# Optimization experiments

Hardware: AMD Instinct MI355X
Metric: run time of the kernel (lower is better)

The kernel has to match this reference:

```python
import jax, jax.numpy as jnp
import numpy as np


def setup_inputs() -> dict:
    key = jax.random.key(0)
    k1, k2 = jax.random.split(key)
    N, D, E = 16384, 4096, 64  # tokens, n_embd, n_exp
    x = jax.random.normal(k1, (N, D), dtype=jnp.float32)
    W = jax.random.normal(k2, (E, D), dtype=jnp.float32) * 0.02  # w_gate weight [n_exp, n_embd]
    return {"x": x, "W": W, "top_k": 4, "n_groups": 8, "n_limited_groups": 4}


def reference(x, W, top_k, n_groups, n_limited_groups):
    ROUTE_SCALE = 1.0
    N = x.shape[0]
    E = W.shape[0]
    exp_per_group = E // n_groups

    logits = x @ W.T                      # [N, E] gate linear (bias=False)
    scores = jax.nn.softmax(logits, -1)   # func == 'softmax'

    # group-limited routing: pick top n_limited_groups groups by max score (bias=False path)
    gs = scores.reshape(N, n_groups, exp_per_group)
    group_scores = gs.max(axis=-1)                             # [N, G]
    _, top_grp = jax.lax.top_k(group_scores, n_limited_groups)  # [N, L]
    selected = jnp.any(
        jnp.arange(n_groups)[None, None, :] == top_grp[:, :, None], axis=1
    )                                                           # [N, G] bool
    masked = jnp.where(selected[:, :, None], gs, -jnp.inf).reshape(N, E)

    # top-k experts over unmasked scores; weights are the gathered scores
    topk_vals, topk_idx = jax.lax.top_k(masked, top_k)          # [N, K]
    weights = (topk_vals * ROUTE_SCALE).astype(x.dtype)         # softmax -> no renorm

    # histc over expert ids
    counts = jnp.zeros((E,), jnp.int32).at[topk_idx.reshape(-1)].add(1)
    return weights, topk_idx, counts
```

## Files before the change

### kernel.cpp

```cpp
#include <hip/hip_runtime.h>
#include <math.h>

#define NTOK 16384
#define DDIM 4096
#define NEXP 64
#define KTOP 4

#define BK   128
#define NSTG (DDIM / BK)
#define TPB  64
#define NBLK (NTOK / TPB)

typedef __attribute__((ext_vector_type(8))) short short8;
typedef __attribute__((ext_vector_type(4))) float f32x4;


__device__ __forceinline__ unsigned short f2bf_rtn(float x) {
    unsigned int b = __float_as_uint(x);
    return (unsigned short)((b + 0x7FFFu + ((b >> 16) & 1u)) >> 16);
}
__device__ __forceinline__ float bf2f(unsigned short h) {
    return __uint_as_float(((unsigned int)h) << 16);
}
__device__ __forceinline__ short8 mk8(unsigned int a, unsigned int b,
                                      unsigned int c, unsigned int d) {
    union { unsigned int u[4]; short8 s; } p;
    p.u[0] = a; p.u[1] = b; p.u[2] = c; p.u[3] = d;
    return p.s;
}
__device__ __forceinline__ void gl2lds16(const void* g, void* l) {
    __builtin_amdgcn_global_load_lds(
        (const __attribute__((address_space(1))) unsigned int*)g,
        (__attribute__((address_space(3))) unsigned int*)l, 16, 0, 0);
}

__global__ __launch_bounds__(256) void prep_kernel(
    const float* __restrict__ W, unsigned short* __restrict__ Whi,
    unsigned short* __restrict__ Wlo, float* __restrict__ counts)
{
    int idx = blockIdx.x * 256 + threadIdx.x;
    float x = W[idx];
    unsigned short h = f2bf_rtn(x);
    float lo = x - bf2f(h);
    Whi[idx] = h;
    Wlo[idx] = f2bf_rtn(lo);
    if (blockIdx.x == 0 && threadIdx.x < NEXP) counts[threadIdx.x] = 0.0f;
}

__global__ __launch_bounds__(512, 2) void gate_kernel(
    const float* __restrict__ X, const unsigned short* __restrict__ Whi,
    const unsigned short* __restrict__ Wlo, float* __restrict__ outW,
    float* __restrict__ outI, float* __restrict__ counts)
{
    __shared__ float          sX[2][TPB * BK];
    __shared__ unsigned short sH[2][NEXP * BK];
    __shared__ unsigned short sL[2][NEXP * BK];
    __shared__ float          lgt[TPB][66];
    __shared__ int            hist[NEXP];

    const int tid  = threadIdx.x;
    const int lane = tid & 63;
    const int w    = tid >> 6;
    const int wm   = w >> 2;
    const int wn   = w & 3;
    const int tok0 = blockIdx.x * TPB;

    if (tid < NEXP) hist[tid] = 0;

    const float* xsrc[4];
    int xdstf[4];
    #pragma unroll
    for (int i = 0; i < 4; ++i) {
        const int seg = w * 4 + i;
        const int r0  = seg * 2 + (lane >> 5);
        const int pc  = lane & 31;
        xsrc[i]  = X + (size_t)(tok0 + r0) * DDIM + ((pc ^ (r0 & 15)) * 4);
        xdstf[i] = seg * 256;
    }
    const unsigned short *whsrc[2], *wlsrc[2];
    int wdsts[2];
    #pragma unroll
    for (int j = 0; j < 2; ++j) {
        const int seg2 = w * 2 + j;
        const int e    = seg2 * 4 + (lane >> 4);
        const int sc   = lane & 15;
        const size_t o = (size_t)e * DDIM + ((sc ^ (e & 15)) * 8);
        whsrc[j] = Whi + o;
        wlsrc[j] = Wlo + o;
        wdsts[j] = seg2 * 512;
    }

    #pragma unroll
    for (int i = 0; i < 4; ++i) gl2lds16(xsrc[i], &sX[0][xdstf[i]]);
    #pragma unroll
    for (int j = 0; j < 2; ++j) {
        gl2lds16(whsrc[j], &sH[0][wdsts[j]]);
        gl2lds16(wlsrc[j], &sL[0][wdsts[j]]);
    }
    __syncthreads();

    const int fr = lane & 15;
    const int fg = lane >> 4;
    const int rowA0 = (wm * 32 + fr) * BK;
    const int rowA1 = rowA0 + 16 * BK;
    const int eB    = (wn * 16 + fr) * BK;

    f32x4 acc[2];
    acc[0] = (f32x4){0.f, 0.f, 0.f, 0.f};
    acc[1] = (f32x4){0.f, 0.f, 0.f, 0.f};

    for (int st = 0; st < NSTG; ++st) {
        const float*          cx = sX[st & 1];
        const unsigned short* ch = sH[st & 1];
        const unsigned short* cl = sL[st & 1];

        if (st + 1 < NSTG) {
            const int nb = (st + 1) & 1;
            const int ko = (st + 1) * BK;
            #pragma unroll
            for (int i = 0; i < 4; ++i)
                gl2lds16(xsrc[i] + ko, &sX[nb][xdstf[i]]);
            #pragma unroll
            for (int j = 0; j < 2; ++j) {
                gl2lds16(whsrc[j] + ko, &sH[nb][wdsts[j]]);
                gl2lds16(wlsrc[j] + ko, &sL[nb][wdsts[j]]);
            }
        }

        #pragma unroll
        for (int ks = 0; ks < 4; ++ks) {
            const int ch0 = ks * 8 + fg * 2;
            const float4 a00 = *(const float4*)&cx[rowA0 + ((ch0     ) ^ fr) * 4];
            const float4 a01 = *(const float4*)&cx[rowA0 + ((ch0 + 1) ^ fr) * 4];
            const float4 a10 = *(const float4*)&cx[rowA1 + ((ch0     ) ^ fr) * 4];
            const float4 a11 = *(const float4*)&cx[rowA1 + ((ch0 + 1) ^ fr) * 4];

            short8 ahi[2], alo[2];
            #pragma unroll
            for (int mg = 0; mg < 2; ++mg) {
                const float4 qa = mg ? a10 : a00;
                const float4 qb = mg ? a11 : a01;
                const unsigned int u0 = __float_as_uint(qa.x), u1 = __float_as_uint(qa.y);
                const unsigned int u2 = __float_as_uint(qa.z), u3 = __float_as_uint(qa.w);
                const unsigned int u4 = __float_as_uint(qb.x), u5 = __float_as_uint(qb.y);
                const unsigned int u6 = __float_as_uint(qb.z), u7 = __float_as_uint(qb.w);
                unsigned int hi0 = (u0 >> 16) | (u1 & 0xFFFF0000u);
                unsigned int hi1 = (u2 >> 16) | (u3 & 0xFFFF0000u);
                unsigned int hi2 = (u4 >> 16) | (u5 & 0xFFFF0000u);
                unsigned int hi3 = (u6 >> 16) | (u7 & 0xFFFF0000u);
                const float l0 = qa.x - __uint_as_float(u0 & 0xFFFF0000u);
                const float l1 = qa.y - __uint_as_float(u1 & 0xFFFF0000u);
                const float l2 = qa.z - __uint_as_float(u2 & 0xFFFF0000u);
                const float l3 = qa.w - __uint_as_float(u3 & 0xFFFF0000u);
                const float l4 = qb.x - __uint_as_float(u4 & 0xFFFF0000u);
                const float l5 = qb.y - __uint_as_float(u5 & 0xFFFF0000u);
                const float l6 = qb.z - __uint_as_float(u6 & 0xFFFF0000u);
                const float l7 = qb.w - __uint_as_float(u7 & 0xFFFF0000u);
                unsigned int lo0 = (__float_as_uint(l0) >> 16) | (__float_as_uint(l1) & 0xFFFF0000u);
                unsigned int lo1 = (__float_as_uint(l2) >> 16) | (__float_as_uint(l3) & 0xFFFF0000u);
                unsigned int lo2 = (__float_as_uint(l4) >> 16) | (__float_as_uint(l5) & 0xFFFF0000u);
                unsigned int lo3 = (__float_as_uint(l6) >> 16) | (__float_as_uint(l7) & 0xFFFF0000u);
                ahi[mg] = mk8(hi0, hi1, hi2, hi3);
                alo[mg] = mk8(lo0, lo1, lo2, lo3);
            }

            const int cb = (ks * 4 + fg) ^ fr;
            const short8 bh = *(const short8*)&ch[eB + cb * 8];
            const short8 bl = *(const short8*)&cl[eB + cb * 8];

            #pragma unroll
            for (int mg = 0; mg < 2; ++mg) {
                acc[mg] = __builtin_amdgcn_mfma_f32_16x16x32_bf16(ahi[mg], bh, acc[mg], 0, 0, 0);
                acc[mg] = __builtin_amdgcn_mfma_f32_16x16x32_bf16(ahi[mg], bl, acc[mg], 0, 0, 0);
                acc[mg] = __builtin_amdgcn_mfma_f32_16x16x32_bf16(alo[mg], bh, acc[mg], 0, 0, 0);
            }
        }

        __syncthreads();
    }

    #pragma unroll
    for (int mg = 0; mg < 2; ++mg)
        #pragma unroll
        for (int r = 0; r < 4; ++r)
            lgt[wm * 32 + mg * 16 + fg * 4 + r][wn * 16 + fr] = acc[mg][r];
    __syncthreads();

    for (int t = 0; t < 8; ++t) {
        const int nl = w * 8 + t;
        const int n  = tok0 + nl;
        const float L = lgt[nl][lane];

        float m = L;
        #pragma unroll
        for (int off = 32; off > 0; off >>= 1) m = fmaxf(m, __shfl_xor(m, off));
        float p = expf(L - m);
        float ssum = p;
        #pragma unroll
        for (int off = 32; off > 0; off >>= 1) ssum += __shfl_xor(ssum, off);
        const float score = p / ssum;

        float gm = score;
        gm = fmaxf(gm, __shfl_xor(gm, 1));
        gm = fmaxf(gm, __shfl_xor(gm, 2));
        gm = fmaxf(gm, __shfl_xor(gm, 4));

        float ga[8];
        #pragma unroll
        for (int g = 0; g < 8; ++g) ga[g] = __shfl(gm, g * 8);
        unsigned selmask = 0u;
        #pragma unroll
        for (int r = 0; r < 4; ++r) {
            float best = -INFINITY; int bg = 0;
            #pragma unroll
            for (int g = 0; g < 8; ++g) {
                bool taken  = (selmask >> g) & 1u;
                bool better = (!taken) && (ga[g] > best);
                bg   = better ? g : bg;
                best = better ? ga[g] : best;
            }
            selmask |= (1u << bg);
        }

        float ms = ((selmask >> (lane >> 3)) & 1u) ? score : -INFINITY;
        float wk[4]; int wi[4];
        #pragma unroll
        for (int r = 0; r < 4; ++r) {
            float v = ms; int ix = lane;
            #pragma unroll
            for (int off = 32; off > 0; off >>= 1) {
                float vo = __shfl_xor(v, off);
                int   io = __shfl_xor(ix, off);
                if (vo > v || (vo == v && io < ix)) { v = vo; ix = io; }
            }
            wk[r] = v; wi[r] = ix;
            if (lane == ix) ms = -INFINITY;
        }

        if (lane == 0) {
            *(float4*)&outW[(size_t)n * 4] = make_float4(wk[0], wk[1], wk[2], wk[3]);
            *(float4*)&outI[(size_t)n * 4] =
                make_float4((float)wi[0], (float)wi[1], (float)wi[2], (float)wi[3]);
            atomicAdd(&hist[wi[0]], 1);
            atomicAdd(&hist[wi[1]], 1);
            atomicAdd(&hist[wi[2]], 1);
            atomicAdd(&hist[wi[3]], 1);
        }
    }

    __syncthreads();
    if (tid < NEXP) atomicAdd(&counts[tid], (float)hist[tid]);
}

extern "C" void kernel_launch(void* const* d_in, const int* in_sizes, int n_in,
                              void* d_out, int out_size, void* d_ws, size_t ws_size,
                              hipStream_t stream) {
    const float* X = (const float*)d_in[0];
    const float* W = (const float*)d_in[1];

    float* outW   = (float*)d_out;
    float* outI   = outW + (size_t)NTOK * KTOP;
    float* counts = outW + (size_t)2 * NTOK * KTOP;

    unsigned short* Whi = (unsigned short*)d_ws;
    unsigned short* Wlo = Whi + (size_t)NEXP * DDIM;

    prep_kernel<<<(NEXP * DDIM) / 256, 256, 0, stream>>>(W, Whi, Wlo, counts);
    gate_kernel<<<NBLK, 512, 0, stream>>>(X, Whi, Wlo, outW, outI, counts);
}
```

Measured before the change: 120.3 us.

## Halve token tile and read bf16 gate weights directly from global memory

The token tile per block shrinks from 64 to 32, and occupancy is raised to four blocks per CU. The split hi/lo bf16 weight tiles are no longer staged through LDS; each lane loads its B fragments straight from global (L2-resident) memory. This frees LDS and cuts the async copy traffic so more blocks can be resident. In exchange, each weight fragment is reused across fewer tokens, and the MFMA loop now depends on global-load latency for B.

Result: slower. 154.4 us (+28.3%).

```diff
diff --git a/kernel.cpp b/kernel.cpp
--- a/kernel.cpp
+++ b/kernel.cpp
@@ -6,10 +6,10 @@
 #define NEXP 64
 #define KTOP 4
 
+#define TPB  32
+#define NBLK (NTOK / TPB)
 #define BK   128
 #define NSTG (DDIM / BK)
-#define TPB  64
-#define NBLK (NTOK / TPB)
 
 typedef __attribute__((ext_vector_type(8))) short short8;
 typedef __attribute__((ext_vector_type(4))) float f32x4;
@@ -47,16 +47,14 @@
     if (blockIdx.x == 0 && threadIdx.x < NEXP) counts[threadIdx.x] = 0.0f;
 }
 
-__global__ __launch_bounds__(512, 2) void gate_kernel(
+__global__ __launch_bounds__(512, 4) void gate_kernel(
     const float* __restrict__ X, const unsigned short* __restrict__ Whi,
     const unsigned short* __restrict__ Wlo, float* __restrict__ outW,
     float* __restrict__ outI, float* __restrict__ counts)
 {
-    __shared__ float          sX[2][TPB * BK];
-    __shared__ unsigned short sH[2][NEXP * BK];
-    __shared__ unsigned short sL[2][NEXP * BK];
-    __shared__ float          lgt[TPB][66];
-    __shared__ int            hist[NEXP];
+    __shared__ float sX[2][TPB * BK];
+    __shared__ float lgt[TPB][66];
+    __shared__ int   hist[NEXP];
 
     const int tid  = threadIdx.x;
     const int lane = tid & 63;
@@ -67,127 +65,86 @@
 
     if (tid < NEXP) hist[tid] = 0;
 
-    const float* xsrc[4];
-    int xdstf[4];
+    const float* xsrc[2];
+    int xdstf[2];
     #pragma unroll
-    for (int i = 0; i < 4; ++i) {
-        const int seg = w * 4 + i;
-        const int r0  = seg * 2 + (lane >> 5);
-        const int pc  = lane & 31;
-        xsrc[i]  = X + (size_t)(tok0 + r0) * DDIM + ((pc ^ (r0 & 15)) * 4);
-        xdstf[i] = seg * 256;
+    for (int i = 0; i < 2; ++i) {
+        const int r = w * 4 + i * 2 + (lane >> 5);
+        const int p = lane & 31;
+        xsrc[i]  = X + (size_t)(tok0 + r) * DDIM + ((p ^ (r & 15)) * 4);
+        xdstf[i] = w * 512 + i * 256;
     }
-    const unsigned short *whsrc[2], *wlsrc[2];
-    int wdsts[2];
-    #pragma unroll
-    for (int j = 0; j < 2; ++j) {
-        const int seg2 = w * 2 + j;
-        const int e    = seg2 * 4 + (lane >> 4);
-        const int sc   = lane & 15;
-        const size_t o = (size_t)e * DDIM + ((sc ^ (e & 15)) * 8);
-        whsrc[j] = Whi + o;
-        wlsrc[j] = Wlo + o;
-        wdsts[j] = seg2 * 512;
-    }
-
-    #pragma unroll
-    for (int i = 0; i < 4; ++i) gl2lds16(xsrc[i], &sX[0][xdstf[i]]);
-    #pragma unroll
-    for (int j = 0; j < 2; ++j) {
-        gl2lds16(whsrc[j], &sH[0][wdsts[j]]);
-        gl2lds16(wlsrc[j], &sL[0][wdsts[j]]);
-    }
+
+    gl2lds16(xsrc[0], &sX[0][xdstf[0]]);
+    gl2lds16(xsrc[1], &sX[0][xdstf[1]]);
     __syncthreads();
 
     const int fr = lane & 15;
     const int fg = lane >> 4;
-    const int rowA0 = (wm * 32 + fr) * BK;
-    const int rowA1 = rowA0 + 16 * BK;
-    const int eB    = (wn * 16 + fr) * BK;
-
-    f32x4 acc[2];
-    acc[0] = (f32x4){0.f, 0.f, 0.f, 0.f};
-    acc[1] = (f32x4){0.f, 0.f, 0.f, 0.f};
+    const int rowA = (wm * 16 + fr) * BK;
+    const unsigned short* wh = Whi + (size_t)(wn * 16 + fr) * DDIM + fg * 8;
+    const unsigned short* wl = Wlo + (size_t)(wn * 16 + fr) * DDIM + fg * 8;
+
+    f32x4 acc = (f32x4){0.f, 0.f, 0.f, 0.f};
 
     for (int st = 0; st < NSTG; ++st) {
-        const float*          cx = sX[st & 1];
-        const unsigned short* ch = sH[st & 1];
-        const unsigned short* cl = sL[st & 1];
+        const float* cx = sX[st & 1];
 
         if (st + 1 < NSTG) {
             const int nb = (st + 1) & 1;
             const int ko = (st + 1) * BK;
-            #pragma unroll
-            for (int i = 0; i < 4; ++i)
-                gl2lds16(xsrc[i] + ko, &sX[nb][xdstf[i]]);
-            #pragma unroll
-            for (int j = 0; j < 2; ++j) {
-                gl2lds16(whsrc[j] + ko, &sH[nb][wdsts[j]]);
-                gl2lds16(wlsrc[j] + ko, &sL[nb][wdsts[j]]);
-            }
+            gl2lds16(xsrc[0] + ko, &sX[nb][xdstf[0]]);
+            gl2lds16(xsrc[1] + ko, &sX[nb][xdstf[1]]);
         }
 
         #pragma unroll
         for (int ks = 0; ks < 4; ++ks) {
-            const int ch0 = ks * 8 + fg * 2;
-            const float4 a00 = *(const float4*)&cx[rowA0 + ((ch0     ) ^ fr) * 4];
-            const float4 a01 = *(const float4*)&cx[rowA0 + ((ch0 + 1) ^ fr) * 4];
-            const float4 a10 = *(const float4*)&cx[rowA1 + ((ch0     ) ^ fr) * 4];
-            const float4 a11 = *(const float4*)&cx[rowA1 + ((ch0 + 1) ^ fr) * 4];
-
-            short8 ahi[2], alo[2];
-            #pragma unroll
-            for (int mg = 0; mg < 2; ++mg) {
-                const float4 qa = mg ? a10 : a00;
-                const float4 qb = mg ? a11 : a01;
-                const unsigned int u0 = __float_as_uint(qa.x), u1 = __float_as_uint(qa.y);
-                const unsigned int u2 = __float_as_uint(qa.z), u3 = __float_as_uint(qa.w);
-                const unsigned int u4 = __float_as_uint(qb.x), u5 = __float_as_uint(qb.y);
-                const unsigned int u6 = __float_as_uint(qb.z), u7 = __float_as_uint(qb.w);
-                unsigned int hi0 = (u0 >> 16) | (u1 & 0xFFFF0000u);
-                unsigned int hi1 = (u2 >> 16) | (u3 & 0xFFFF0000u);
-                unsigned int hi2 = (u4 >> 16) | (u5 & 0xFFFF0000u);
-                unsigned int hi3 = (u6 >> 16) | (u7 & 0xFFFF0000u);
-                const float l0 = qa.x - __uint_as_float(u0 & 0xFFFF0000u);
-                const float l1 = qa.y - __uint_as_float(u1 & 0xFFFF0000u);
-                const float l2 = qa.z - __uint_as_float(u2 & 0xFFFF0000u);
-                const float l3 = qa.w - __uint_as_float(u3 & 0xFFFF0000u);
-                const float l4 = qb.x - __uint_as_float(u4 & 0xFFFF0000u);
-                const float l5 = qb.y - __uint_as_float(u5 & 0xFFFF0000u);
-                const float l6 = qb.z - __uint_as_float(u6 & 0xFFFF0000u);
-                const float l7 = qb.w - __uint_as_float(u7 & 0xFFFF0000u);
-                unsigned int lo0 = (__float_as_uint(l0) >> 16) | (__float_as_uint(l1) & 0xFFFF0000u);
-                unsigned int lo1 = (__float_as_uint(l2) >> 16) | (__float_as_uint(l3) & 0xFFFF0000u);
-                unsigned int lo2 = (__float_as_uint(l4) >> 16) | (__float_as_uint(l5) & 0xFFFF0000u);
-                unsigned int lo3 = (__float_as_uint(l6) >> 16) | (__float_as_uint(l7) & 0xFFFF0000u);
-                ahi[mg] = mk8(hi0, hi1, hi2, hi3);
-                alo[mg] = mk8(lo0, lo1, lo2, lo3);
-            }
-
-            const int cb = (ks * 4 + fg) ^ fr;
-            const short8 bh = *(const short8*)&ch[eB + cb * 8];
-            const short8 bl = *(const short8*)&cl[eB + cb * 8];
-
-            #pragma unroll
-            for (int mg = 0; mg < 2; ++mg) {
-                acc[mg] = __builtin_amdgcn_mfma_f32_16x16x32_bf16(ahi[mg], bh, acc[mg], 0, 0, 0);
-                acc[mg] = __builtin_amdgcn_mfma_f32_16x16x32_bf16(ahi[mg], bl, acc[mg], 0, 0, 0);
-                acc[mg] = __builtin_amdgcn_mfma_f32_16x16x32_bf16(alo[mg], bh, acc[mg], 0, 0, 0);
-            }
+            const int ko = st * BK + ks * 32;
+            const short8 bh = *(const short8*)(wh + ko);
+            const short8 bl = *(const short8*)(wl + ko);
+
+            const int c0 = ks * 8 + fg * 2;
+            const float4 qa = *(const float4*)&cx[rowA + ((c0    ) ^ fr) * 4];
+            const float4 qb = *(const float4*)&cx[rowA + ((c0 + 1) ^ fr) * 4];
+
+            const unsigned int u0 = __float_as_uint(qa.x), u1 = __float_as_uint(qa.y);
+            const unsigned int u2 = __float_as_uint(qa.z), u3 = __float_as_uint(qa.w);
+            const unsigned int u4 = __float_as_uint(qb.x), u5 = __float_as_uint(qb.y);
+            const unsigned int u6 = __float_as_uint(qb.z), u7 = __float_as_uint(qb.w);
+            const unsigned int hi0 = (u0 >> 16) | (u1 & 0xFFFF0000u);
+            const unsigned int hi1 = (u2 >> 16) | (u3 & 0xFFFF0000u);
+            const unsigned int hi2 = (u4 >> 16) | (u5 & 0xFFFF0000u);
+            const unsigned int hi3 = (u6 >> 16) | (u7 & 0xFFFF0000u);
+            const float l0 = qa.x - __uint_as_float(u0 & 0xFFFF0000u);
+            const float l1 = qa.y - __uint_as_float(u1 & 0xFFFF0000u);
+            const float l2 = qa.z - __uint_as_float(u2 & 0xFFFF0000u);
+            const float l3 = qa.w - __uint_as_float(u3 & 0xFFFF0000u);
+            const float l4 = qb.x - __uint_as_float(u4 & 0xFFFF0000u);
+            const float l5 = qb.y - __uint_as_float(u5 & 0xFFFF0000u);
+            const float l6 = qb.z - __uint_as_float(u6 & 0xFFFF0000u);
+            const float l7 = qb.w - __uint_as_float(u7 & 0xFFFF0000u);
+            const unsigned int lo0 = (__float_as_uint(l0) >> 16) | (__float_as_uint(l1) & 0xFFFF0000u);
+            const unsigned int lo1 = (__float_as_uint(l2) >> 16) | (__float_as_uint(l3) & 0xFFFF0000u);
+            const unsigned int lo2 = (__float_as_uint(l4) >> 16) | (__float_as_uint(l5) & 0xFFFF0000u);
+            const unsigned int lo3 = (__float_as_uint(l6) >> 16) | (__float_as_uint(l7) & 0xFFFF0000u);
+            const short8 ahi = mk8(hi0, hi1, hi2, hi3);
+            const short8 alo = mk8(lo0, lo1, lo2, lo3);
+
+            acc = __builtin_amdgcn_mfma_f32_16x16x32_bf16(ahi, bh, acc, 0, 0, 0);
+            acc = __builtin_amdgcn_mfma_f32_16x16x32_bf16(ahi, bl, acc, 0, 0, 0);
+            acc = __builtin_amdgcn_mfma_f32_16x16x32_bf16(alo, bh, acc, 0, 0, 0);
         }
 
         __syncthreads();
     }
 
     #pragma unroll
-    for (int mg = 0; mg < 2; ++mg)
-        #pragma unroll
-        for (int r = 0; r < 4; ++r)
-            lgt[wm * 32 + mg * 16 + fg * 4 + r][wn * 16 + fr] = acc[mg][r];
+    for (int r = 0; r < 4; ++r)
+        lgt[wm * 16 + fg * 4 + r][wn * 16 + fr] = acc[r];
     __syncthreads();
 
-    for (int t = 0; t < 8; ++t) {
-        const int nl = w * 8 + t;
+    for (int t = 0; t < 4; ++t) {
+        const int nl = w * 4 + t;
         const int n  = tok0 + nl;
         const float L = lgt[nl][lane];
 
```
